# Performance work log

Measured on AMD Instinct MI355X. Metric: run time of the kernel, lower is better.

The kernel has to match this reference:

```python
import jax, jax.numpy as jnp
import numpy as np

DIM = 1024
NUM_HEADS = 16
HEAD_DIM = DIM // NUM_HEADS
SCALE = HEAD_DIM ** (-0.5)


def setup_inputs() -> dict:
    key = jax.random.key(0)
    ks = jax.random.split(key, 5)
    b, n = 4, 1370
    x = jax.random.normal(ks[0], (b, n, DIM), dtype=jnp.float32)
    # Dense kernels: Keras Dense stores kernel as [in, out]
    w_qkv = jax.random.normal(ks[1], (DIM, 3 * DIM), dtype=jnp.float32) * (DIM ** -0.5)
    b_qkv = jnp.zeros((3 * DIM,), dtype=jnp.float32)
    w_proj = jax.random.normal(ks[2], (DIM, DIM), dtype=jnp.float32) * (DIM ** -0.5)
    b_proj = jnp.zeros((DIM,), dtype=jnp.float32)
    return {"x": x, "w_qkv": w_qkv, "b_qkv": b_qkv, "w_proj": w_proj, "b_proj": b_proj}


def reference(x, w_qkv, b_qkv, w_proj, b_proj):
    b, n, _ = x.shape
    qkv = x @ w_qkv + b_qkv                       # [b, n, 3*dim]
    qkv = qkv.reshape(b, n, 3, NUM_HEADS, HEAD_DIM)
    qkv = jnp.transpose(qkv, (2, 0, 3, 1, 4))     # [3, b, h, n, d]
    q, k, v = qkv[0], qkv[1], qkv[2]
    q = q * jnp.asarray(SCALE, dtype=q.dtype)
    attn = jnp.einsum("bhqd,bhkd->bhqk", q, k)    # [b, h, n, n]
    attn = jax.nn.softmax(attn, axis=-1)
    out = jnp.einsum("bhqk,bhkd->bhqd", attn, v)  # [b, h, n, d]
    out = jnp.transpose(out, (0, 2, 1, 3)).reshape(b, n, DIM)
    return out @ w_proj + b_proj
```

## Files before the change

kernel.cpp:

```cpp
#include <hip/hip_runtime.h>
#include <stdint.h>
#include <math.h>

typedef __attribute__((ext_vector_type(8))) __bf16 bf16x8;
typedef __attribute__((ext_vector_type(4))) __bf16 bf16x4;
typedef __attribute__((ext_vector_type(4))) float f32x4;
typedef __attribute__((ext_vector_type(8))) short short8;

#define MFMA(a, b, c) __builtin_amdgcn_mfma_f32_16x16x32_bf16((a), (b), (c), 0, 0, 0)

constexpr int DIMC  = 1024;
constexpr int HEADS = 16;
constexpr int HD    = 64;
constexpr int BATCH = 4;
constexpr int SEQ   = 1370;
constexpr int MROWS = BATCH * SEQ;
constexpr int NPAD  = 1408;
constexpr float QK_SCALE = 0.125f * 1.44269504088896341f;

__device__ __forceinline__ unsigned short f2bf(float f) {
    union { float f; unsigned int u; } v; v.f = f;
    unsigned int r = (v.u + 0x7FFFu + ((v.u >> 16) & 1u)) >> 16;
    return (unsigned short)r;
}

__device__ __forceinline__ void gl2lds16(const unsigned short* g, unsigned short* l) {
    __builtin_amdgcn_global_load_lds(
        (const __attribute__((address_space(1))) unsigned int*)g,
        (__attribute__((address_space(3))) unsigned int*)l,
        16, 0, 0);
}

__device__ __forceinline__ void transpose_tile(const float* __restrict__ in,
                                               unsigned short* __restrict__ out,
                                               int R, int C, int cb, int rb) {
    __shared__ float tile[32][33];
    int tx = threadIdx.x & 31, ty = threadIdx.x >> 5;
    int cbase = cb * 32, rbase = rb * 32;
#pragma unroll
    for (int rr = 0; rr < 4; ++rr) {
        int r = ty + rr * 8;
        tile[r][tx] = in[(size_t)(rbase + r) * C + cbase + tx];
    }
    __syncthreads();
#pragma unroll
    for (int rr = 0; rr < 4; ++rr) {
        int cr = ty + rr * 8;
        out[(size_t)(cbase + cr) * R + rbase + tx] = f2bf(tile[tx][cr]);
    }
}

__global__ __launch_bounds__(256) void prep_kernel(const float* __restrict__ x,
                                                   unsigned short* __restrict__ xb,
                                                   const float* __restrict__ w_qkv,
                                                   unsigned short* __restrict__ wqkvT,
                                                   const float* __restrict__ w_proj,
                                                   unsigned short* __restrict__ wprojT,
                                                   unsigned short* __restrict__ vTg) {
    int bid = blockIdx.x;
    if (bid < 2740) {
        int i = bid * 256 + threadIdx.x;
        f32x4 a = reinterpret_cast<const f32x4*>(x)[2 * i];
        f32x4 b = reinterpret_cast<const f32x4*>(x)[2 * i + 1];
        short8 o;
        o[0] = (short)f2bf(a[0]); o[1] = (short)f2bf(a[1]);
        o[2] = (short)f2bf(a[2]); o[3] = (short)f2bf(a[3]);
        o[4] = (short)f2bf(b[0]); o[5] = (short)f2bf(b[1]);
        o[6] = (short)f2bf(b[2]); o[7] = (short)f2bf(b[3]);
        reinterpret_cast<short8*>(xb)[i] = o;
    } else if (bid < 2740 + 3072) {
        int b = bid - 2740;
        transpose_tile(w_qkv, wqkvT, 1024, 3072, b % 96, b / 96);
    } else if (bid < 2740 + 3072 + 1024) {
        int b = bid - (2740 + 3072);
        transpose_tile(w_proj, wprojT, 1024, 1024, b % 32, b / 32);
    } else {
        int idx = (bid - 6836) * 256 + threadIdx.x;
        const int padw = NPAD - SEQ;
        int col = SEQ + idx % padw;
        int rowflat = idx / padw;
        vTg[(size_t)rowflat * NPAD + col] = 0;
    }
}

template <int EPI>
__global__ __launch_bounds__(512) void gemm_bt_kernel(const unsigned short* __restrict__ A,
                                                      const unsigned short* __restrict__ Bt,
                                                      int M, int N, int K, int Nx,
                                                      const float* __restrict__ bias,
                                                      unsigned short* __restrict__ qg,
                                                      unsigned short* __restrict__ kg,
                                                      unsigned short* __restrict__ vTg,
                                                      float* __restrict__ outf) {
    __shared__ unsigned short As[2][128 * 32];
    __shared__ unsigned short Bs[2][128 * 32];
    const int tid = threadIdx.x;
    const int l = tid & 63, w = tid >> 6;
    const int wr = w >> 2, wc = w & 3;
    const int lm = l & 15, lk = l >> 4;

    int nwg = gridDim.x;
    int wgid = (blockIdx.x & 7) * (nwg >> 3) + (blockIdx.x >> 3);
    int bx = wgid % Nx, by = wgid / Nx;
    const int brow = by * 128, bcol = bx * 128;

    f32x4 acc[4][2];
#pragma unroll
    for (int i = 0; i < 4; ++i)
#pragma unroll
        for (int j = 0; j < 2; ++j) acc[i][j] = f32x4{0.f, 0.f, 0.f, 0.f};

    const int srow = tid >> 2;
    const int ssrc = (((tid & 3) ^ ((srow >> 1) & 3)) << 3);
    auto stage = [&](int kt, int buf) {
        int ga = min(brow + srow, M - 1);
        gl2lds16(&A[(size_t)ga * K + kt * 32 + ssrc], &As[buf][tid * 8]);
        int gb = bcol + srow;
        gl2lds16(&Bt[(size_t)gb * K + kt * 32 + ssrc], &Bs[buf][tid * 8]);
    };

    const int nkt = K >> 5;
    stage(0, 0);
    __syncthreads();
    int cur = 0;
    for (int kt = 0; kt < nkt; ++kt) {
        if (kt + 1 < nkt) stage(kt + 1, cur ^ 1);

        const int swa = (lk ^ ((lm >> 1) & 3)) * 8;
        bf16x8 af[4], bfr[2];
#pragma unroll
        for (int i = 0; i < 4; ++i)
            af[i] = *reinterpret_cast<const bf16x8*>(&As[cur][(wr * 64 + i * 16 + lm) * 32 + swa]);
#pragma unroll
        for (int j = 0; j < 2; ++j)
            bfr[j] = *reinterpret_cast<const bf16x8*>(&Bs[cur][(wc * 32 + j * 16 + lm) * 32 + swa]);
        __builtin_amdgcn_s_setprio(1);
#pragma unroll
        for (int i = 0; i < 4; ++i)
#pragma unroll
            for (int j = 0; j < 2; ++j)
                acc[i][j] = MFMA(af[i], bfr[j], acc[i][j]);
        __builtin_amdgcn_s_setprio(0);
        __syncthreads();
        cur ^= 1;
    }

#pragma unroll
    for (int i = 0; i < 4; ++i) {
        int mbase = brow + wr * 64 + i * 16 + lk * 4;
#pragma unroll
        for (int j = 0; j < 2; ++j) {
            int col = bcol + wc * 32 + j * 16 + lm;
            float bv = bias[col];
#pragma unroll
            for (int r = 0; r < 4; ++r) {
                int m = mbase + r;
                if (m >= M) continue;
                float val = acc[i][j][r] + bv;
                if constexpr (EPI == 0) {
                    int which = col >> 10;
                    int head = (col >> 6) & 15;
                    int d = col & 63;
                    int b = m / SEQ;
                    int nseq = m - b * SEQ;
                    int bh = b * HEADS + head;
                    if (which == 0) {
                        qg[((size_t)bh * SEQ + nseq) * HD + d] = f2bf(val * QK_SCALE);
                    } else if (which == 1) {
                        kg[((size_t)bh * SEQ + nseq) * HD + d] = f2bf(val);
                    } else {
                        vTg[((size_t)bh * HD + d) * NPAD + nseq] = f2bf(val);
                    }
                } else {
                    outf[(size_t)m * DIMC + col] = val;
                }
            }
        }
    }
}

__global__ __launch_bounds__(512) void attn_kernel(const unsigned short* __restrict__ qg,
                                                   const unsigned short* __restrict__ kg,
                                                   const unsigned short* __restrict__ vTg,
                                                   unsigned short* __restrict__ ao) {
    __shared__ unsigned short Ks[64 * 72];
    __shared__ unsigned short Vs[64 * 72];
    __shared__ unsigned short Pw[8][16 * 72];

    const int tid = threadIdx.x;
    const int l = tid & 63, w = tid >> 6;
    const int lm = l & 15, lk = l >> 4;

    int wg = (blockIdx.x & 7) * 88 + (blockIdx.x >> 3);
    const int bh = wg / 11;
    const int qbase = (wg - bh * 11) * 128;

    int qr = min(qbase + w * 16 + lm, SEQ - 1);
    const unsigned short* qp = &qg[((size_t)bh * SEQ + qr) * HD + lk * 8];
    bf16x8 qf0 = *reinterpret_cast<const bf16x8*>(qp);
    bf16x8 qf1 = *reinterpret_cast<const bf16x8*>(qp + 32);

    f32x4 o[4];
#pragma unroll
    for (int jd = 0; jd < 4; ++jd) o[jd] = f32x4{0.f, 0.f, 0.f, 0.f};
    float mrun = -INFINITY, lrun = 0.f;

    const int r0 = tid >> 3;
    const int c8b = (tid & 7) << 3;
    const unsigned short* kbase = &kg[(size_t)bh * SEQ * HD];
    const unsigned short* vbase = &vTg[(size_t)bh * HD * NPAD];

    short8 kr, vr;
    auto load_tile = [&](int t) {
        int kvg = min(t * 64 + r0, SEQ - 1);
        kr = *reinterpret_cast<const short8*>(&kbase[(size_t)kvg * HD + c8b]);
        vr = *reinterpret_cast<const short8*>(&vbase[(size_t)r0 * NPAD + t * 64 + c8b]);
    };
    auto write_tile = [&]() {
        *reinterpret_cast<short8*>(&Ks[r0 * 72 + c8b]) = kr;
        *reinterpret_cast<short8*>(&Vs[r0 * 72 + c8b]) = vr;
    };

    const int NT = (SEQ + 63) >> 6;
    load_tile(0);
    for (int t = 0; t < NT; ++t) {
        write_tile();
        __syncthreads();
        if (t + 1 < NT) load_tile(t + 1);

        f32x4 s[4];
        __builtin_amdgcn_s_setprio(1);
#pragma unroll
        for (int j = 0; j < 4; ++j) {
            f32x4 z = {0.f, 0.f, 0.f, 0.f};
            bf16x8 k0 = *reinterpret_cast<const bf16x8*>(&Ks[(j * 16 + lm) * 72 + lk * 8]);
            bf16x8 k1 = *reinterpret_cast<const bf16x8*>(&Ks[(j * 16 + lm) * 72 + 32 + lk * 8]);
            z = MFMA(k0, qf0, z);
            z = MFMA(k1, qf1, z);
            s[j] = z;
        }
        __builtin_amdgcn_s_setprio(0);

        if (t == NT - 1) {
#pragma unroll
            for (int j = 0; j < 4; ++j)
#pragma unroll
                for (int r = 0; r < 4; ++r) {
                    int kvg = t * 64 + j * 16 + lk * 4 + r;
                    if (kvg >= SEQ) s[j][r] = -INFINITY;
                }
        }

        float tmax = s[0][0];
#pragma unroll
        for (int j = 0; j < 4; ++j)
#pragma unroll
            for (int r = 0; r < 4; ++r) tmax = fmaxf(tmax, s[j][r]);

        if (!__all(tmax - mrun <= 8.0f)) {
            float tm = fmaxf(tmax, __shfl_xor(tmax, 16));
            tm = fmaxf(tm, __shfl_xor(tm, 32));
            float mnew = fmaxf(mrun, tm);
            float scale = exp2f(mrun - mnew);
            mrun = mnew;
            lrun *= scale;
            float sc[4];
#pragma unroll
            for (int r = 0; r < 4; ++r) sc[r] = __shfl(scale, lk * 4 + r);
#pragma unroll
            for (int jd = 0; jd < 4; ++jd) {
                o[jd][0] *= sc[0]; o[jd][1] *= sc[1];
                o[jd][2] *= sc[2]; o[jd][3] *= sc[3];
            }
        }

        float p[4][4];
        float psum = 0.f;
#pragma unroll
        for (int j = 0; j < 4; ++j)
#pragma unroll
            for (int r = 0; r < 4; ++r) {
                float pv = exp2f(s[j][r] - mrun);
                p[j][r] = pv;
                psum += pv;
            }
        lrun += psum;

#pragma unroll
        for (int j = 0; j < 4; ++j) {
            bf16x4 pk;
            pk[0] = (__bf16)p[j][0]; pk[1] = (__bf16)p[j][1];
            pk[2] = (__bf16)p[j][2]; pk[3] = (__bf16)p[j][3];
            *reinterpret_cast<bf16x4*>(&Pw[w][lm * 72 + j * 16 + lk * 4]) = pk;
        }

        bf16x8 pa0 = *reinterpret_cast<const bf16x8*>(&Pw[w][lm * 72 + lk * 8]);
        bf16x8 pa1 = *reinterpret_cast<const bf16x8*>(&Pw[w][lm * 72 + 32 + lk * 8]);
        __builtin_amdgcn_s_setprio(1);
#pragma unroll
        for (int jd = 0; jd < 4; ++jd) {
            bf16x8 v0 = *reinterpret_cast<const bf16x8*>(&Vs[(jd * 16 + lm) * 72 + lk * 8]);
            bf16x8 v1 = *reinterpret_cast<const bf16x8*>(&Vs[(jd * 16 + lm) * 72 + 32 + lk * 8]);
            o[jd] = MFMA(pa0, v0, o[jd]);
            o[jd] = MFMA(pa1, v1, o[jd]);
        }
        __builtin_amdgcn_s_setprio(0);
        __syncthreads();
    }

    float ltot = lrun;
    ltot += __shfl_xor(ltot, 16);
    ltot += __shfl_xor(ltot, 32);
    float linv = 1.f / ltot;
    int b = bh >> 4, h = bh & 15;
#pragma unroll
    for (int r = 0; r < 4; ++r) {
        int q = qbase + w * 16 + lk * 4 + r;
        float inv = __shfl(linv, lk * 4 + r);
        if (q >= SEQ) continue;
#pragma unroll
        for (int jd = 0; jd < 4; ++jd) {
            ao[((size_t)b * SEQ + q) * DIMC + h * HD + jd * 16 + lm] = f2bf(o[jd][r] * inv);
        }
    }
}

extern "C" void kernel_launch(void* const* d_in, const int* in_sizes, int n_in,
                              void* d_out, int out_size, void* d_ws, size_t ws_size,
                              hipStream_t stream) {
    const float* x      = (const float*)d_in[0];
    const float* w_qkv  = (const float*)d_in[1];
    const float* b_qkv  = (const float*)d_in[2];
    const float* w_proj = (const float*)d_in[3];
    const float* b_proj = (const float*)d_in[4];
    float* out = (float*)d_out;

    char* ws = (char*)d_ws;
    unsigned short* xb     = (unsigned short*)ws; ws += (size_t)MROWS * DIMC * 2;
    unsigned short* wqkvT  = (unsigned short*)ws; ws += (size_t)3 * DIMC * DIMC * 2;
    unsigned short* wprojT = (unsigned short*)ws; ws += (size_t)DIMC * DIMC * 2;
    unsigned short* qg     = (unsigned short*)ws; ws += (size_t)64 * SEQ * HD * 2;
    unsigned short* kg     = (unsigned short*)ws; ws += (size_t)64 * SEQ * HD * 2;
    unsigned short* vTg    = (unsigned short*)ws; ws += (size_t)64 * HD * NPAD * 2;
    unsigned short* ao     = (unsigned short*)ws; ws += (size_t)MROWS * DIMC * 2;

    prep_kernel<<<dim3(7444), 256, 0, stream>>>(x, xb, w_qkv, wqkvT, w_proj, wprojT, vTg);

    gemm_bt_kernel<0><<<dim3(24 * 43), 512, 0, stream>>>(
        xb, wqkvT, MROWS, 3 * DIMC, DIMC, 24, b_qkv, qg, kg, vTg, nullptr);

    attn_kernel<<<dim3(8 * 88), 512, 0, stream>>>(qg, kg, vTg, ao);

    gemm_bt_kernel<1><<<dim3(8 * 43), 512, 0, stream>>>(
        ao, wprojT, MROWS, DIMC, DIMC, 8, b_proj, nullptr, nullptr, nullptr, out);
}
```

Baseline: 172.5 us.

## Give the QKV projection a dedicated GEMM with 128x256x64 tiles and XOR-swizzled LDS

Splits the templated GEMM into a QKV-specific kernel and a plain output-projection kernel. The QKV kernel uses larger 128x256 output tiles with a 64-deep K step, so each wave holds a 4x4 MFMA accumulator block and reuses its loaded fragments more often. It also XOR-swizzles LDS rows to avoid bank conflicts, and prefetches two stages ahead with explicit vmcnt waits. The goal is less global and LDS traffic per FLOP in the largest GEMM. The costs are about 96KB of LDS per block and more registers per thread, which may limit occupancy, and 516 blocks may leave the 256 CUs unevenly loaded.

```diff
diff --git a/kernel.cpp b/kernel.cpp
--- a/kernel.cpp
+++ b/kernel.cpp
@@ -83,15 +83,128 @@
     }
 }
 
-template <int EPI>
-__global__ __launch_bounds__(512) void gemm_bt_kernel(const unsigned short* __restrict__ A,
-                                                      const unsigned short* __restrict__ Bt,
-                                                      int M, int N, int K, int Nx,
-                                                      const float* __restrict__ bias,
-                                                      unsigned short* __restrict__ qg,
-                                                      unsigned short* __restrict__ kg,
-                                                      unsigned short* __restrict__ vTg,
-                                                      float* __restrict__ outf) {
+__global__ __launch_bounds__(512, 2) void gemm_qkv_kernel(const unsigned short* __restrict__ A,
+                                                          const unsigned short* __restrict__ Bt,
+                                                          int M, int N, int K,
+                                                          const float* __restrict__ bias,
+                                                          unsigned short* __restrict__ qg,
+                                                          unsigned short* __restrict__ kg,
+                                                          unsigned short* __restrict__ vTg) {
+    __shared__ unsigned short As[2][128 * 64];
+    __shared__ unsigned short Bs[2][256 * 64];
+    const int tid = threadIdx.x;
+    const int l = tid & 63, w = tid >> 6;
+    const int wr = w & 1, wc = w >> 1;
+    const int lm = l & 15, lk = l >> 4;
+
+    const int bx = blockIdx.x % 12, by = blockIdx.x / 12;
+    const int brow = by * 128, bcol = bx * 256;
+
+    f32x4 acc[4][4];
+#pragma unroll
+    for (int i = 0; i < 4; ++i)
+#pragma unroll
+        for (int j = 0; j < 4; ++j) acc[i][j] = f32x4{0.f, 0.f, 0.f, 0.f};
+
+    auto stage = [&](int kt, int buf) {
+#pragma unroll
+        for (int q = 0; q < 2; ++q) {
+            int cid = q * 512 + tid;
+            int row = cid >> 3, kc = cid & 7;
+            int src = ((kc ^ (row & 7)) << 3);
+            int ga = min(brow + row, M - 1);
+            gl2lds16(&A[(size_t)ga * K + kt * 64 + src], &As[buf][cid * 8]);
+        }
+#pragma unroll
+        for (int q = 0; q < 4; ++q) {
+            int cid = q * 512 + tid;
+            int row = cid >> 3, kc = cid & 7;
+            int src = ((kc ^ (row & 7)) << 3);
+            int gb = bcol + row;
+            gl2lds16(&Bt[(size_t)gb * K + kt * 64 + src], &Bs[buf][cid * 8]);
+        }
+    };
+
+    const int nkt = K >> 6;
+    stage(0, 0);
+    stage(1, 1);
+    asm volatile("s_waitcnt vmcnt(6)" ::: "memory");
+    __builtin_amdgcn_s_barrier();
+
+    for (int kt = 0; kt < nkt; ++kt) {
+        const int cur = kt & 1;
+        bf16x8 af[4][2], bfr[4][2];
+#pragma unroll
+        for (int i = 0; i < 4; ++i)
+#pragma unroll
+            for (int ks = 0; ks < 2; ++ks) {
+                int row = wr * 64 + i * 16 + lm;
+                int slot = (ks * 4 + lk) ^ (lm & 7);
+                af[i][ks] = *reinterpret_cast<const bf16x8*>(&As[cur][row * 64 + slot * 8]);
+            }
+#pragma unroll
+        for (int j = 0; j < 4; ++j)
+#pragma unroll
+            for (int ks = 0; ks < 2; ++ks) {
+                int row = wc * 64 + j * 16 + lm;
+                int slot = (ks * 4 + lk) ^ (lm & 7);
+                bfr[j][ks] = *reinterpret_cast<const bf16x8*>(&Bs[cur][row * 64 + slot * 8]);
+            }
+        __builtin_amdgcn_s_setprio(1);
+#pragma unroll
+        for (int i = 0; i < 4; ++i)
+#pragma unroll
+            for (int j = 0; j < 4; ++j)
+#pragma unroll
+                for (int ks = 0; ks < 2; ++ks)
+                    acc[i][j] = MFMA(af[i][ks], bfr[j][ks], acc[i][j]);
+        __builtin_amdgcn_s_setprio(0);
+
+        __builtin_amdgcn_s_barrier();
+        if (kt + 2 < nkt) {
+            stage(kt + 2, cur);
+            asm volatile("s_waitcnt vmcnt(6)" ::: "memory");
+        } else if (kt + 1 < nkt) {
+            asm volatile("s_waitcnt vmcnt(0)" ::: "memory");
+        }
+        if (kt + 1 < nkt) __builtin_amdgcn_s_barrier();
+    }
+
+#pragma unroll
+    for (int i = 0; i < 4; ++i) {
+        int mbase = brow + wr * 64 + i * 16 + lk * 4;
+#pragma unroll
+        for (int j = 0; j < 4; ++j) {
+            int col = bcol + wc * 64 + j * 16 + lm;
+            float bv = bias[col];
+            int which = col >> 10;
+            int head = (col >> 6) & 15;
+            int d = col & 63;
+#pragma unroll
+            for (int r = 0; r < 4; ++r) {
+                int m = mbase + r;
+                if (m >= M) continue;
+                float val = acc[i][j][r] + bv;
+                int b = m / SEQ;
+                int nseq = m - b * SEQ;
+                int bh = b * HEADS + head;
+                if (which == 0) {
+                    qg[((size_t)bh * SEQ + nseq) * HD + d] = f2bf(val * QK_SCALE);
+                } else if (which == 1) {
+                    kg[((size_t)bh * SEQ + nseq) * HD + d] = f2bf(val);
+                } else {
+                    vTg[((size_t)bh * HD + d) * NPAD + nseq] = f2bf(val);
+                }
+            }
+        }
+    }
+}
+
+__global__ __launch_bounds__(512) void gemm_proj_kernel(const unsigned short* __restrict__ A,
+                                                        const unsigned short* __restrict__ Bt,
+                                                        int M, int N, int K, int Nx,
+                                                        const float* __restrict__ bias,
+                                                        float* __restrict__ outf) {
     __shared__ unsigned short As[2][128 * 32];
     __shared__ unsigned short Bs[2][128 * 32];
     const int tid = threadIdx.x;
@@ -156,24 +269,7 @@
             for (int r = 0; r < 4; ++r) {
                 int m = mbase + r;
                 if (m >= M) continue;
-                float val = acc[i][j][r] + bv;
-                if constexpr (EPI == 0) {
-                    int which = col >> 10;
-                    int head = (col >> 6) & 15;
-                    int d = col & 63;
-                    int b = m / SEQ;
-                    int nseq = m - b * SEQ;
-                    int bh = b * HEADS + head;
-                    if (which == 0) {
-                        qg[((size_t)bh * SEQ + nseq) * HD + d] = f2bf(val * QK_SCALE);
-                    } else if (which == 1) {
-                        kg[((size_t)bh * SEQ + nseq) * HD + d] = f2bf(val);
-                    } else {
-                        vTg[((size_t)bh * HD + d) * NPAD + nseq] = f2bf(val);
-                    }
-                } else {
-                    outf[(size_t)m * DIMC + col] = val;
-                }
+                outf[(size_t)m * DIMC + col] = acc[i][j][r] + bv;
             }
         }
     }
@@ -346,11 +442,11 @@
 
     prep_kernel<<<dim3(7444), 256, 0, stream>>>(x, xb, w_qkv, wqkvT, w_proj, wprojT, vTg);
 
-    gemm_bt_kernel<0><<<dim3(24 * 43), 512, 0, stream>>>(
-        xb, wqkvT, MROWS, 3 * DIMC, DIMC, 24, b_qkv, qg, kg, vTg, nullptr);
+    gemm_qkv_kernel<<<dim3(43 * 12), 512, 0, stream>>>(
+        xb, wqkvT, MROWS, 3 * DIMC, DIMC, b_qkv, qg, kg, vTg);
 
     attn_kernel<<<dim3(8 * 88), 512, 0, stream>>>(qg, kg, vTg, ao);
 
-    gemm_bt_kernel<1><<<dim3(8 * 43), 512, 0, stream>>>(
-        ao, wprojT, MROWS, DIMC, DIMC, 8, b_proj, nullptr, nullptr, nullptr, out);
-}
+    gemm_proj_kernel<<<dim3(8 * 43), 512, 0, stream>>>(
+        ao, wprojT, MROWS, DIMC, DIMC, 8, b_proj, out);
+}
```

Measured after the change: 200.8 us. +16.4%, slower.
